# Performance work log

Hardware: AMD Instinct MI355X
Metric: run time of the kernel (lower is better)

Reference implementation:

```python
import jax, jax.numpy as jnp
import numpy as np

S, B, HQ, HKV, D = 2048, 2, 32, 8, 128
SCALE = 1.0 / np.sqrt(D).astype(np.float32)  # scale_factor = 1/sqrt(head_dim)


def setup_inputs() -> dict:
    key = jax.random.key(0)
    kq, kk, kv = jax.random.split(key, 3)
    return {
        "query": jax.random.normal(kq, (S, B, HQ, D), dtype=jnp.float32),
        "key": jax.random.normal(kk, (S, B, HKV, D), dtype=jnp.float32),
        "value": jax.random.normal(kv, (S, B, HKV, D), dtype=jnp.float32),
    }


def reference(query, key, value):
    # GQA: reshape query into [S, B, h_kv, group, D]
    group = HQ // HKV
    gq = query.reshape(S, B, HKV, group, D)
    # logits: [B, h_kv, group, Sq, Sk]
    logits = jnp.einsum("qbhgd,kbhd->bhgqk", gq, key) * jnp.float32(SCALE)
    # scaled upper-triangular (causal) masked softmax
    causal = jnp.tril(jnp.ones((S, S), dtype=bool))  # allow k <= q
    logits = jnp.where(causal[None, None, None], logits, jnp.finfo(jnp.float32).min)
    attn = jax.nn.softmax(logits, axis=-1)
    out = jnp.einsum("bhgqk,kbhd->qbhgd", attn, value)
    return out.reshape(S, B, HQ, D)
```

## Files before the change

kernel.cpp:

```cpp
#include <hip/hip_runtime.h>

#define SEQ    2048
#define BATCH  2
#define NHQ    32
#define NHKV   8
#define DHEAD  128
#define QSCALE2 0.12751743f

typedef __fp16 f16;
typedef f16 f16x2 __attribute__((ext_vector_type(2)));
typedef f16 f16x4 __attribute__((ext_vector_type(4)));
typedef f16 f16x8 __attribute__((ext_vector_type(8)));
typedef float f32x4 __attribute__((ext_vector_type(4)));

#define KSTRIDE 136
#define VSTRIDE 40
#define KBUF    (32 * KSTRIDE)
#define VBUF    (128 * VSTRIDE)

static __device__ __forceinline__ float fast_exp2(float x) {
#if __has_builtin(__builtin_amdgcn_exp2f)
  return __builtin_amdgcn_exp2f(x);
#else
  return __builtin_exp2f(x);
#endif
}

__global__ __launch_bounds__(512, 4) void attn_fwd(const float* __restrict__ Q,
                                                   const float* __restrict__ K,
                                                   const float* __restrict__ V,
                                                   float* __restrict__ O) {
  const int bh     = (int)blockIdx.x * 8 + ((int)blockIdx.y >> 3);
  const int pair_i = (int)blockIdx.y & 7;
  const int b   = bh >> 5;
  const int hq  = bh & 31;
  const int hkv = hq >> 2;
  const int t    = threadIdx.x;
  const int wave = t >> 6;
  const int lane = t & 63;
  const int col  = lane & 15;
  const int quad = lane >> 4;

  const int qrs = BATCH * NHQ * DHEAD;
  const int krs = BATCH * NHKV * DHEAD;

  const float* Qp = Q + ((size_t)b * NHQ  + hq ) * DHEAD;
  const float* Kp = K + ((size_t)b * NHKV + hkv) * DHEAD;
  const float* Vp = V + ((size_t)b * NHKV + hkv) * DHEAD;
  float*       Op = O + ((size_t)b * NHQ  + hq ) * DHEAD;

  __shared__ __align__(16) f16 smem[2 * KBUF + 2 * VBUF];

  const int ktk = t >> 5;
  const int ktd = (t & 31) * 4;
  const int vd  = t & 127;
  const int vh  = t >> 7;
  const int klr = ((ktk >> 2) & 1) * 16 + (ktk >> 3) * 4 + (ktk & 3);

  #pragma unroll 1
  for (int pass = 0; pass < 2; ++pass) {
    const int qt     = pass ? pair_i : 15 - pair_i;
    const int q_base = qt * 128 + wave * 16;

    f16x8 qf[4];
    {
      const float* qsrc = Qp + (size_t)(q_base + col) * qrs + quad * 8;
      #pragma unroll
      for (int c = 0; c < 4; ++c) {
        float4 a = *(const float4*)(qsrc + c * 32);
        float4 e = *(const float4*)(qsrc + c * 32 + 4);
        f16x2 p0 = __builtin_amdgcn_cvt_pkrtz(a.x * QSCALE2, a.y * QSCALE2);
        f16x2 p1 = __builtin_amdgcn_cvt_pkrtz(a.z * QSCALE2, a.w * QSCALE2);
        f16x2 p2 = __builtin_amdgcn_cvt_pkrtz(e.x * QSCALE2, e.y * QSCALE2);
        f16x2 p3 = __builtin_amdgcn_cvt_pkrtz(e.z * QSCALE2, e.w * QSCALE2);
        qf[c][0] = p0[0]; qf[c][1] = p0[1]; qf[c][2] = p1[0]; qf[c][3] = p1[1];
        qf[c][4] = p2[0]; qf[c][5] = p2[1]; qf[c][6] = p3[0]; qf[c][7] = p3[1];
      }
    }

    f32x4 oacc[8];
    #pragma unroll
    for (int h = 0; h < 8; ++h) oacc[h] = (f32x4){0.f, 0.f, 0.f, 0.f};
    float m_i = -__builtin_inff();
    float l_i = 0.f;

    const int nt_blk = 4 * qt + 4;
    const int nt_w   = 4 * qt + (wave >> 1) + 1;

    float4 kr[2];
    float  vf[8];

    #pragma unroll
    for (int ro = 0; ro < 2; ++ro)
      kr[ro] = *(const float4*)(Kp + (size_t)(ktk + ro * 16) * krs + ktd);
    #pragma unroll
    for (int i = 0; i < 8; ++i)
      vf[i] = Vp[(size_t)(vh * 8 + i) * krs + vd];

    for (int kt = 0; kt < nt_blk; ++kt) {
      const int bf = kt & 1;
      f16* kb = smem + bf * KBUF;
      f16* vb = smem + 2 * KBUF + bf * VBUF;

      #pragma unroll
      for (int ro = 0; ro < 2; ++ro) {
        f16x2 lo = __builtin_amdgcn_cvt_pkrtz(kr[ro].x, kr[ro].y);
        f16x2 hi = __builtin_amdgcn_cvt_pkrtz(kr[ro].z, kr[ro].w);
        f16x4 v4; v4[0] = lo[0]; v4[1] = lo[1]; v4[2] = hi[0]; v4[3] = hi[1];
        *(f16x4*)(kb + (klr + ro * 8) * KSTRIDE + ktd) = v4;
      }
      {
        f16x2 p0 = __builtin_amdgcn_cvt_pkrtz(vf[0], vf[1]);
        f16x2 p1 = __builtin_amdgcn_cvt_pkrtz(vf[2], vf[3]);
        f16x2 p2 = __builtin_amdgcn_cvt_pkrtz(vf[4], vf[5]);
        f16x2 p3 = __builtin_amdgcn_cvt_pkrtz(vf[6], vf[7]);
        f16x8 v8;
        v8[0] = p0[0]; v8[1] = p0[1]; v8[2] = p1[0]; v8[3] = p1[1];
        v8[4] = p2[0]; v8[5] = p2[1]; v8[6] = p3[0]; v8[7] = p3[1];
        *(f16x8*)(vb + vd * VSTRIDE + vh * 8) = v8;
      }

      if (kt + 1 < nt_blk) {
        const int k0n = (kt + 1) * 32;
        #pragma unroll
        for (int ro = 0; ro < 2; ++ro)
          kr[ro] = *(const float4*)(Kp + (size_t)(k0n + ktk + ro * 16) * krs + ktd);
        #pragma unroll
        for (int i = 0; i < 8; ++i)
          vf[i] = Vp[(size_t)(k0n + vh * 8 + i) * krs + vd];
      }

      __syncthreads();

      if (kt < nt_w) {
        const int k0 = kt * 32;

        f32x4 s0 = {0.f, 0.f, 0.f, 0.f}, s1 = {0.f, 0.f, 0.f, 0.f};
        __builtin_amdgcn_s_setprio(1);
        #pragma unroll
        for (int c = 0; c < 4; ++c) {
          f16x8 ka = *(const f16x8*)(kb + col * KSTRIDE + quad * 8 + c * 32);
          s0 = __builtin_amdgcn_mfma_f32_16x16x32_f16(ka, qf[c], s0, 0, 0, 0);
        }
        #pragma unroll
        for (int c = 0; c < 4; ++c) {
          f16x8 ka = *(const f16x8*)(kb + (16 + col) * KSTRIDE + quad * 8 + c * 32);
          s1 = __builtin_amdgcn_mfma_f32_16x16x32_f16(ka, qf[c], s1, 0, 0, 0);
        }
        __builtin_amdgcn_s_setprio(0);

        const int qrow = q_base + col;
        if (k0 + 31 > q_base) {
          #pragma unroll
          for (int r = 0; r < 4; ++r) {
            if (k0 + quad * 8 + r     > qrow) s0[r] = -__builtin_inff();
            if (k0 + quad * 8 + 4 + r > qrow) s1[r] = -__builtin_inff();
          }
        }

        float mx = fmaxf(fmaxf(fmaxf(s0[0], s0[1]), fmaxf(s0[2], s0[3])),
                         fmaxf(fmaxf(s1[0], s1[1]), fmaxf(s1[2], s1[3])));
        mx = fmaxf(mx, __shfl_xor(mx, 16, 64));
        mx = fmaxf(mx, __shfl_xor(mx, 32, 64));

        if (!__all(mx - m_i <= 8.0f)) {
          const float mnew  = fmaxf(m_i, mx);
          const float alpha = fast_exp2(m_i - mnew);
          m_i = mnew;
          l_i *= alpha;
          #pragma unroll
          for (int h = 0; h < 8; ++h) {
            oacc[h][0] *= alpha; oacc[h][1] *= alpha;
            oacc[h][2] *= alpha; oacc[h][3] *= alpha;
          }
        }

        float e0[4], e1[4], rs = 0.f;
        #pragma unroll
        for (int r = 0; r < 4; ++r) {
          e0[r] = fast_exp2(s0[r] - m_i);
          e1[r] = fast_exp2(s1[r] - m_i);
          rs += e0[r] + e1[r];
        }
        l_i += rs;

        f16x2 a01 = __builtin_amdgcn_cvt_pkrtz(e0[0], e0[1]);
        f16x2 a23 = __builtin_amdgcn_cvt_pkrtz(e0[2], e0[3]);
        f16x2 b01 = __builtin_amdgcn_cvt_pkrtz(e1[0], e1[1]);
        f16x2 b23 = __builtin_amdgcn_cvt_pkrtz(e1[2], e1[3]);
        f16x8 pb;
        pb[0] = a01[0]; pb[1] = a01[1]; pb[2] = a23[0]; pb[3] = a23[1];
        pb[4] = b01[0]; pb[5] = b01[1]; pb[6] = b23[0]; pb[7] = b23[1];

        __builtin_amdgcn_s_setprio(1);
        #pragma unroll
        for (int h = 0; h < 8; ++h) {
          f16x8 va = *(const f16x8*)(vb + (h * 16 + col) * VSTRIDE + quad * 8);
          oacc[h] = __builtin_amdgcn_mfma_f32_16x16x32_f16(va, pb, oacc[h], 0, 0, 0);
        }
        __builtin_amdgcn_s_setprio(0);
      }
    }

    {
      float lt = l_i + __shfl_xor(l_i, 16, 64);
      lt += __shfl_xor(lt, 32, 64);
      const float invl = 1.0f / lt;
      #pragma unroll
      for (int h = 0; h < 8; ++h) {
        float4 o;
        o.x = oacc[h][0] * invl; o.y = oacc[h][1] * invl;
        o.z = oacc[h][2] * invl; o.w = oacc[h][3] * invl;
        *(float4*)(Op + (size_t)(q_base + col) * qrs + h * 16 + quad * 4) = o;
      }
    }
  }
}

extern "C" void kernel_launch(void* const* d_in, const int* in_sizes, int n_in,
                              void* d_out, int out_size, void* d_ws, size_t ws_size,
                              hipStream_t stream) {
  const float* Q = (const float*)d_in[0];
  const float* K = (const float*)d_in[1];
  const float* V = (const float*)d_in[2];
  float* O = (float*)d_out;
  (void)in_sizes; (void)n_in; (void)out_size; (void)d_ws; (void)ws_size;
  dim3 grid(SEQ / 256, BATCH * NHQ);
  attn_fwd<<<grid, dim3(512), 0, stream>>>(Q, K, V, O);
}
```

Before: 228.8 us.

## Stage 64-key K/V tiles per barrier and sum probabilities with fdot2

Each shared-memory stage now holds 64 keys instead of 32, processed as two 32-key sub-tiles per __syncthreads, which halves the number of block-wide barriers and global-load rounds. More registers hold prefetched K/V (kr[4], vf[16]), and LDS use grows (KBUF doubles and VSTRIDE rises to 72). The row-sum of probabilities now comes from the f16-packed values via fdot2 against ones instead of separate fp32 adds, and the max reduction is reassociated. The extra register and LDS pressure may reduce occupancy under launch_bounds(512,4).

Measured after the change: 252.4 us. +10.3%, slower.

```diff
diff --git a/kernel.cpp b/kernel.cpp
--- a/kernel.cpp
+++ b/kernel.cpp
@@ -14,8 +14,8 @@
 typedef float f32x4 __attribute__((ext_vector_type(4)));
 
 #define KSTRIDE 136
-#define VSTRIDE 40
-#define KBUF    (32 * KSTRIDE)
+#define VSTRIDE 72
+#define KBUF    (64 * KSTRIDE)
 #define VBUF    (128 * VSTRIDE)
 
 static __device__ __forceinline__ float fast_exp2(float x) {
@@ -57,6 +57,8 @@
   const int vh  = t >> 7;
   const int klr = ((ktk >> 2) & 1) * 16 + (ktk >> 3) * 4 + (ktk & 3);
 
+  const f16x2 kOne = {(f16)1.f, (f16)1.f};
+
   #pragma unroll 1
   for (int pass = 0; pass < 2; ++pass) {
     const int qt     = pass ? pair_i : 15 - pair_i;
@@ -84,121 +86,144 @@
     float m_i = -__builtin_inff();
     float l_i = 0.f;
 
-    const int nt_blk = 4 * qt + 4;
-    const int nt_w   = 4 * qt + (wave >> 1) + 1;
-
-    float4 kr[2];
-    float  vf[8];
+    const int nt2  = 2 * qt + 2;
+    const int nt_w = 4 * qt + (wave >> 1) + 1;
+
+    float4 kr[4];
+    float  vf[16];
 
     #pragma unroll
-    for (int ro = 0; ro < 2; ++ro)
+    for (int ro = 0; ro < 4; ++ro)
       kr[ro] = *(const float4*)(Kp + (size_t)(ktk + ro * 16) * krs + ktd);
     #pragma unroll
-    for (int i = 0; i < 8; ++i)
-      vf[i] = Vp[(size_t)(vh * 8 + i) * krs + vd];
-
-    for (int kt = 0; kt < nt_blk; ++kt) {
-      const int bf = kt & 1;
+    for (int i = 0; i < 8; ++i) {
+      vf[i]     = Vp[(size_t)(vh * 8 + i) * krs + vd];
+      vf[8 + i] = Vp[(size_t)(vh * 8 + i + 32) * krs + vd];
+    }
+
+    for (int kt2 = 0; kt2 < nt2; ++kt2) {
+      const int bf = kt2 & 1;
       f16* kb = smem + bf * KBUF;
       f16* vb = smem + 2 * KBUF + bf * VBUF;
 
       #pragma unroll
-      for (int ro = 0; ro < 2; ++ro) {
+      for (int ro = 0; ro < 4; ++ro) {
         f16x2 lo = __builtin_amdgcn_cvt_pkrtz(kr[ro].x, kr[ro].y);
         f16x2 hi = __builtin_amdgcn_cvt_pkrtz(kr[ro].z, kr[ro].w);
         f16x4 v4; v4[0] = lo[0]; v4[1] = lo[1]; v4[2] = hi[0]; v4[3] = hi[1];
-        *(f16x4*)(kb + (klr + ro * 8) * KSTRIDE + ktd) = v4;
-      }
-      {
-        f16x2 p0 = __builtin_amdgcn_cvt_pkrtz(vf[0], vf[1]);
-        f16x2 p1 = __builtin_amdgcn_cvt_pkrtz(vf[2], vf[3]);
-        f16x2 p2 = __builtin_amdgcn_cvt_pkrtz(vf[4], vf[5]);
-        f16x2 p3 = __builtin_amdgcn_cvt_pkrtz(vf[6], vf[7]);
+        *(f16x4*)(kb + ((ro >> 1) * 32 + klr + (ro & 1) * 8) * KSTRIDE + ktd) = v4;
+      }
+      #pragma unroll
+      for (int g = 0; g < 2; ++g) {
+        f16x2 p0 = __builtin_amdgcn_cvt_pkrtz(vf[g * 8 + 0], vf[g * 8 + 1]);
+        f16x2 p1 = __builtin_amdgcn_cvt_pkrtz(vf[g * 8 + 2], vf[g * 8 + 3]);
+        f16x2 p2 = __builtin_amdgcn_cvt_pkrtz(vf[g * 8 + 4], vf[g * 8 + 5]);
+        f16x2 p3 = __builtin_amdgcn_cvt_pkrtz(vf[g * 8 + 6], vf[g * 8 + 7]);
         f16x8 v8;
         v8[0] = p0[0]; v8[1] = p0[1]; v8[2] = p1[0]; v8[3] = p1[1];
         v8[4] = p2[0]; v8[5] = p2[1]; v8[6] = p3[0]; v8[7] = p3[1];
-        *(f16x8*)(vb + vd * VSTRIDE + vh * 8) = v8;
-      }
-
-      if (kt + 1 < nt_blk) {
-        const int k0n = (kt + 1) * 32;
+        *(f16x8*)(vb + vd * VSTRIDE + g * 32 + vh * 8) = v8;
+      }
+
+      if (kt2 + 1 < nt2) {
+        const int k0n = (kt2 + 1) * 64;
         #pragma unroll
-        for (int ro = 0; ro < 2; ++ro)
+        for (int ro = 0; ro < 4; ++ro)
           kr[ro] = *(const float4*)(Kp + (size_t)(k0n + ktk + ro * 16) * krs + ktd);
         #pragma unroll
-        for (int i = 0; i < 8; ++i)
-          vf[i] = Vp[(size_t)(k0n + vh * 8 + i) * krs + vd];
+        for (int i = 0; i < 8; ++i) {
+          vf[i]     = Vp[(size_t)(k0n + vh * 8 + i) * krs + vd];
+          vf[8 + i] = Vp[(size_t)(k0n + vh * 8 + i + 32) * krs + vd];
+        }
       }
 
       __syncthreads();
 
-      if (kt < nt_w) {
-        const int k0 = kt * 32;
-
-        f32x4 s0 = {0.f, 0.f, 0.f, 0.f}, s1 = {0.f, 0.f, 0.f, 0.f};
-        __builtin_amdgcn_s_setprio(1);
-        #pragma unroll
-        for (int c = 0; c < 4; ++c) {
-          f16x8 ka = *(const f16x8*)(kb + col * KSTRIDE + quad * 8 + c * 32);
-          s0 = __builtin_amdgcn_mfma_f32_16x16x32_f16(ka, qf[c], s0, 0, 0, 0);
+      #pragma unroll
+      for (int s = 0; s < 2; ++s) {
+        const int sub = kt2 * 2 + s;
+        if (sub < nt_w) {
+          const int k0 = sub * 32;
+          const f16* kbs = kb + (s * 32) * KSTRIDE;
+
+          f32x4 s0 = {0.f, 0.f, 0.f, 0.f}, s1 = {0.f, 0.f, 0.f, 0.f};
+          __builtin_amdgcn_s_setprio(1);
+          #pragma unroll
+          for (int c = 0; c < 4; ++c) {
+            f16x8 ka = *(const f16x8*)(kbs + col * KSTRIDE + quad * 8 + c * 32);
+            s0 = __builtin_amdgcn_mfma_f32_16x16x32_f16(ka, qf[c], s0, 0, 0, 0);
+          }
+          #pragma unroll
+          for (int c = 0; c < 4; ++c) {
+            f16x8 ka = *(const f16x8*)(kbs + (16 + col) * KSTRIDE + quad * 8 + c * 32);
+            s1 = __builtin_amdgcn_mfma_f32_16x16x32_f16(ka, qf[c], s1, 0, 0, 0);
+          }
+          __builtin_amdgcn_s_setprio(0);
+
+          const int qrow = q_base + col;
+          if (k0 + 31 > q_base) {
+            #pragma unroll
+            for (int r = 0; r < 4; ++r) {
+              if (k0 + quad * 8 + r     > qrow) s0[r] = -__builtin_inff();
+              if (k0 + quad * 8 + 4 + r > qrow) s1[r] = -__builtin_inff();
+            }
+          }
+
+          float m1 = fmaxf(fmaxf(s0[0], s0[1]), s0[2]);
+          float m2 = fmaxf(fmaxf(s0[3], s1[0]), s1[1]);
+          float m3 = fmaxf(fmaxf(s1[2], s1[3]), m1);
+          float mx = fmaxf(m2, m3);
+          mx = fmaxf(mx, __shfl_xor(mx, 16, 64));
+          mx = fmaxf(mx, __shfl_xor(mx, 32, 64));
+
+          if (!__all(mx - m_i <= 8.0f)) {
+            const float mnew  = fmaxf(m_i, mx);
+            const float alpha = fast_exp2(m_i - mnew);
+            m_i = mnew;
+            l_i *= alpha;
+            #pragma unroll
+            for (int h = 0; h < 8; ++h) {
+              oacc[h][0] *= alpha; oacc[h][1] *= alpha;
+              oacc[h][2] *= alpha; oacc[h][3] *= alpha;
+            }
+          }
+
+          float e0[4], e1[4];
+          #pragma unroll
+          for (int r = 0; r < 4; ++r) {
+            e0[r] = fast_exp2(s0[r] - m_i);
+            e1[r] = fast_exp2(s1[r] - m_i);
+          }
+
+          f16x2 a01 = __builtin_amdgcn_cvt_pkrtz(e0[0], e0[1]);
+          f16x2 a23 = __builtin_amdgcn_cvt_pkrtz(e0[2], e0[3]);
+          f16x2 b01 = __builtin_amdgcn_cvt_pkrtz(e1[0], e1[1]);
+          f16x2 b23 = __builtin_amdgcn_cvt_pkrtz(e1[2], e1[3]);
+          f16x8 pb;
+          pb[0] = a01[0]; pb[1] = a01[1]; pb[2] = a23[0]; pb[3] = a23[1];
+          pb[4] = b01[0]; pb[5] = b01[1]; pb[6] = b23[0]; pb[7] = b23[1];
+
+#if __has_builtin(__builtin_amdgcn_fdot2)
+          float rs = __builtin_amdgcn_fdot2(a01, kOne,
+                       __builtin_amdgcn_fdot2(a23, kOne,
+                         __builtin_amdgcn_fdot2(b01, kOne,
+                           __builtin_amdgcn_fdot2(b23, kOne, 0.f, false),
+                           false), false), false);
+#else
+          float rs = 0.f;
+          #pragma unroll
+          for (int r = 0; r < 4; ++r) rs += e0[r] + e1[r];
+#endif
+          l_i += rs;
+
+          __builtin_amdgcn_s_setprio(1);
+          #pragma unroll
+          for (int h = 0; h < 8; ++h) {
+            f16x8 va = *(const f16x8*)(vb + (h * 16 + col) * VSTRIDE + s * 32 + quad * 8);
+            oacc[h] = __builtin_amdgcn_mfma_f32_16x16x32_f16(va, pb, oacc[h], 0, 0, 0);
+          }
+          __builtin_amdgcn_s_setprio(0);
         }
-        #pragma unroll
-        for (int c = 0; c < 4; ++c) {
-          f16x8 ka = *(const f16x8*)(kb + (16 + col) * KSTRIDE + quad * 8 + c * 32);
-          s1 = __builtin_amdgcn_mfma_f32_16x16x32_f16(ka, qf[c], s1, 0, 0, 0);
-        }
-        __builtin_amdgcn_s_setprio(0);
-
-        const int qrow = q_base + col;
-        if (k0 + 31 > q_base) {
-          #pragma unroll
-          for (int r = 0; r < 4; ++r) {
-            if (k0 + quad * 8 + r     > qrow) s0[r] = -__builtin_inff();
-            if (k0 + quad * 8 + 4 + r > qrow) s1[r] = -__builtin_inff();
-          }
-        }
-
-        float mx = fmaxf(fmaxf(fmaxf(s0[0], s0[1]), fmaxf(s0[2], s0[3])),
-                         fmaxf(fmaxf(s1[0], s1[1]), fmaxf(s1[2], s1[3])));
-        mx = fmaxf(mx, __shfl_xor(mx, 16, 64));
-        mx = fmaxf(mx, __shfl_xor(mx, 32, 64));
-
-        if (!__all(mx - m_i <= 8.0f)) {
-          const float mnew  = fmaxf(m_i, mx);
-          const float alpha = fast_exp2(m_i - mnew);
-          m_i = mnew;
-          l_i *= alpha;
-          #pragma unroll
-          for (int h = 0; h < 8; ++h) {
-            oacc[h][0] *= alpha; oacc[h][1] *= alpha;
-            oacc[h][2] *= alpha; oacc[h][3] *= alpha;
-          }
-        }
-
-        float e0[4], e1[4], rs = 0.f;
-        #pragma unroll
-        for (int r = 0; r < 4; ++r) {
-          e0[r] = fast_exp2(s0[r] - m_i);
-          e1[r] = fast_exp2(s1[r] - m_i);
-          rs += e0[r] + e1[r];
-        }
-        l_i += rs;
-
-        f16x2 a01 = __builtin_amdgcn_cvt_pkrtz(e0[0], e0[1]);
-        f16x2 a23 = __builtin_amdgcn_cvt_pkrtz(e0[2], e0[3]);
-        f16x2 b01 = __builtin_amdgcn_cvt_pkrtz(e1[0], e1[1]);
-        f16x2 b23 = __builtin_amdgcn_cvt_pkrtz(e1[2], e1[3]);
-        f16x8 pb;
-        pb[0] = a01[0]; pb[1] = a01[1]; pb[2] = a23[0]; pb[3] = a23[1];
-        pb[4] = b01[0]; pb[5] = b01[1]; pb[6] = b23[0]; pb[7] = b23[1];
-
-        __builtin_amdgcn_s_setprio(1);
-        #pragma unroll
-        for (int h = 0; h < 8; ++h) {
-          f16x8 va = *(const f16x8*)(vb + (h * 16 + col) * VSTRIDE + quad * 8);
-          oacc[h] = __builtin_amdgcn_mfma_f32_16x16x32_f16(va, pb, oacc[h], 0, 0, 0);
-        }
-        __builtin_amdgcn_s_setprio(0);
       }
     }
 
```
